# Kernel optimization log

Hardware: AMD Instinct MI355X
Metric: run time of the kernel (lower is better)

## Reference

```python
import jax, jax.numpy as jnp
import numpy as np

EMB_BOUND = 0.000316
T, E, D = 16, 100000, 128
B = 4096
L = 20  # fixed bag length used to build offsets (TBE supports ragged; math identical)


def setup_inputs() -> dict:
    key = jax.random.key(0)
    kw, ki = jax.random.split(key)
    weights = jax.random.uniform(kw, (T, E, D), dtype=jnp.float32,
                                 minval=-EMB_BOUND, maxval=EMB_BOUND)
    indices = jax.random.randint(ki, (T * B * L,), 0, E, dtype=jnp.int64)
    offsets = (jnp.arange(T * B + 1, dtype=jnp.int64) * L)
    return {"weights": weights, "indices": indices, "offsets": offsets}


def reference(weights, indices, offsets):
    # weights: [T, E, D]; indices: [N] flat; offsets: [T*B+1], table-major bags.
    n = indices.shape[0]
    num_bags = offsets.shape[0] - 1  # T*B
    b = num_bags // T
    # bag (segment) id for each lookup index
    seg = jnp.searchsorted(offsets, jnp.arange(n, dtype=offsets.dtype), side='right') - 1
    table = seg // b  # which table each lookup belongs to
    flat_w = weights.reshape(T * E, D)
    rows = flat_w[table * E + indices]  # [N, D] irregular gather
    pooled = jax.ops.segment_sum(rows, seg, num_segments=num_bags)  # [T*B, D]
    # table-major -> [B, T*D]
    return pooled.reshape(T, b, D).transpose(1, 0, 2).reshape(b, T * D)
```

## Files before the change

### kernel.cpp

```cpp
#include <hip/hip_runtime.h>


constexpr int T = 16;
constexpr int E = 100000;
constexpr int D = 128;
constexpr int BAGS_PER_TABLE = 4096;
constexpr int NUM_BAGS = T * BAGS_PER_TABLE;
constexpr int WAVES_PER_BLOCK = 4;

__global__ __launch_bounds__(256) void tbe_pool_kernel(
    const float* __restrict__ weights,
    const int* __restrict__ indices,
    const int* __restrict__ offsets,
    float* __restrict__ out)
{
    const int wave = threadIdx.x >> 6;
    const int lane = threadIdx.x & 63;
    const int bag  = blockIdx.x * WAVES_PER_BLOCK + wave;
    if (bag >= NUM_BAGS) return;

    const int t = bag / BAGS_PER_TABLE;
    const int b = bag - t * BAGS_PER_TABLE;

    const int start = offsets[bag];
    const int end   = offsets[bag + 1];

    const float2* __restrict__ tbl =
        reinterpret_cast<const float2*>(weights + (long long)t * E * D);

    float2 a0 = {0.f, 0.f}, a1 = {0.f, 0.f}, a2 = {0.f, 0.f}, a3 = {0.f, 0.f};

    int i = start;
    for (; i + 4 <= end; i += 4) {
        const int i0 = indices[i];
        const int i1 = indices[i + 1];
        const int i2 = indices[i + 2];
        const int i3 = indices[i + 3];
        const float2 v0 = tbl[(long long)i0 * (D / 2) + lane];
        const float2 v1 = tbl[(long long)i1 * (D / 2) + lane];
        const float2 v2 = tbl[(long long)i2 * (D / 2) + lane];
        const float2 v3 = tbl[(long long)i3 * (D / 2) + lane];
        a0.x += v0.x; a0.y += v0.y;
        a1.x += v1.x; a1.y += v1.y;
        a2.x += v2.x; a2.y += v2.y;
        a3.x += v3.x; a3.y += v3.y;
    }
    for (; i < end; ++i) {
        const int i0 = indices[i];
        const float2 v0 = tbl[(long long)i0 * (D / 2) + lane];
        a0.x += v0.x; a0.y += v0.y;
    }

    float2 acc;
    acc.x = (a0.x + a1.x) + (a2.x + a3.x);
    acc.y = (a0.y + a1.y) + (a2.y + a3.y);

    float2* __restrict__ o =
        reinterpret_cast<float2*>(out + (long long)b * (T * D) + t * D);
    o[lane] = acc;
}

extern "C" void kernel_launch(void* const* d_in, const int* in_sizes, int n_in,
                              void* d_out, int out_size, void* d_ws, size_t ws_size,
                              hipStream_t stream) {
    const float* weights = (const float*)d_in[0];
    const int*   indices = (const int*)d_in[1];
    const int*   offsets = (const int*)d_in[2];
    float*       out     = (float*)d_out;

    const int grid = NUM_BAGS / WAVES_PER_BLOCK;
    tbe_pool_kernel<<<grid, 256, 0, stream>>>(weights, indices, offsets, out);
}
```

Baseline: 969.8 us.

## Gather two rows per wave with 16-byte loads and shuffle-broadcast indices

Each wave now splits into two 32-lane halves, and each half gathers a different embedding row with 16-byte vector loads, so one wave instruction fetches two rows. Bag indices are read cooperatively once per 64 and broadcast with shuffles instead of per-lane scalar loads. The halves are combined with a cross-half shuffle reduction, and output is written with nontemporal stores. Row offsets use 32-bit unsigned byte arithmetic, which fits within one table, in exchange for the extra shuffle work and reduction.

```diff
diff --git a/kernel.cpp b/kernel.cpp
--- a/kernel.cpp
+++ b/kernel.cpp
@@ -7,6 +7,10 @@
 constexpr int BAGS_PER_TABLE = 4096;
 constexpr int NUM_BAGS = T * BAGS_PER_TABLE;
 constexpr int WAVES_PER_BLOCK = 4;
+constexpr int BLOCKS_PER_TABLE = BAGS_PER_TABLE / WAVES_PER_BLOCK;
+static_assert(BAGS_PER_TABLE % WAVES_PER_BLOCK == 0, "table must be block-aligned");
+
+typedef float f4 __attribute__((ext_vector_type(4)));
 
 __global__ __launch_bounds__(256) void tbe_pool_kernel(
     const float* __restrict__ weights,
@@ -16,48 +20,69 @@
 {
     const int wave = threadIdx.x >> 6;
     const int lane = threadIdx.x & 63;
-    const int bag  = blockIdx.x * WAVES_PER_BLOCK + wave;
-    if (bag >= NUM_BAGS) return;
+    const int half = lane >> 5;
+    const int l32  = lane & 31;
 
-    const int t = bag / BAGS_PER_TABLE;
-    const int b = bag - t * BAGS_PER_TABLE;
+    const int t            = blockIdx.x / BLOCKS_PER_TABLE;
+    const int bag_in_table = (blockIdx.x % BLOCKS_PER_TABLE) * WAVES_PER_BLOCK + wave;
+    const int bag          = t * BAGS_PER_TABLE + bag_in_table;
 
     const int start = offsets[bag];
     const int end   = offsets[bag + 1];
 
-    const float2* __restrict__ tbl =
-        reinterpret_cast<const float2*>(weights + (long long)t * E * D);
+    const char* __restrict__ tbl =
+        reinterpret_cast<const char*>(weights) + (size_t)t * E * D * sizeof(float);
+    const unsigned laneByte = (unsigned)(l32 * 16);
 
-    float2 a0 = {0.f, 0.f}, a1 = {0.f, 0.f}, a2 = {0.f, 0.f}, a3 = {0.f, 0.f};
+    f4 a0 = {0.f, 0.f, 0.f, 0.f};
+    f4 a1 = {0.f, 0.f, 0.f, 0.f};
+    f4 a2 = {0.f, 0.f, 0.f, 0.f};
+    f4 a3 = {0.f, 0.f, 0.f, 0.f};
 
-    int i = start;
-    for (; i + 4 <= end; i += 4) {
-        const int i0 = indices[i];
-        const int i1 = indices[i + 1];
-        const int i2 = indices[i + 2];
-        const int i3 = indices[i + 3];
-        const float2 v0 = tbl[(long long)i0 * (D / 2) + lane];
-        const float2 v1 = tbl[(long long)i1 * (D / 2) + lane];
-        const float2 v2 = tbl[(long long)i2 * (D / 2) + lane];
-        const float2 v3 = tbl[(long long)i3 * (D / 2) + lane];
-        a0.x += v0.x; a0.y += v0.y;
-        a1.x += v1.x; a1.y += v1.y;
-        a2.x += v2.x; a2.y += v2.y;
-        a3.x += v3.x; a3.y += v3.y;
-    }
-    for (; i < end; ++i) {
-        const int i0 = indices[i];
-        const float2 v0 = tbl[(long long)i0 * (D / 2) + lane];
-        a0.x += v0.x; a0.y += v0.y;
+    for (int base = start; base < end; base += 64) {
+        const int navail = min(64, end - base);
+
+        int myidx = 0;
+        if (lane < navail) myidx = indices[base + lane];
+
+        const int npairs = navail >> 1;
+        int p = 0;
+        for (; p + 4 <= npairs; p += 4) {
+            const int r0 = __shfl(myidx, 2 * (p + 0) + half);
+            const int r1 = __shfl(myidx, 2 * (p + 1) + half);
+            const int r2 = __shfl(myidx, 2 * (p + 2) + half);
+            const int r3 = __shfl(myidx, 2 * (p + 3) + half);
+            const f4 v0 = *reinterpret_cast<const f4*>(tbl + ((unsigned)r0 * 512u + laneByte));
+            const f4 v1 = *reinterpret_cast<const f4*>(tbl + ((unsigned)r1 * 512u + laneByte));
+            const f4 v2 = *reinterpret_cast<const f4*>(tbl + ((unsigned)r2 * 512u + laneByte));
+            const f4 v3 = *reinterpret_cast<const f4*>(tbl + ((unsigned)r3 * 512u + laneByte));
+            a0 += v0; a1 += v1; a2 += v2; a3 += v3;
+        }
+        for (; p < npairs; ++p) {
+            const int r0 = __shfl(myidx, 2 * p + half);
+            const f4 v0 = *reinterpret_cast<const f4*>(tbl + ((unsigned)r0 * 512u + laneByte));
+            a0 += v0;
+        }
+        if (navail & 1) {
+            const int r0 = __shfl(myidx, navail - 1);
+            if (half == 0) {
+                const f4 v0 = *reinterpret_cast<const f4*>(tbl + ((unsigned)r0 * 512u + laneByte));
+                a0 += v0;
+            }
+        }
     }
 
-    float2 acc;
-    acc.x = (a0.x + a1.x) + (a2.x + a3.x);
-    acc.y = (a0.y + a1.y) + (a2.y + a3.y);
+    f4 acc = (a0 + a1) + (a2 + a3);
+    acc.x += __shfl_xor(acc.x, 32);
+    acc.y += __shfl_xor(acc.y, 32);
+    acc.z += __shfl_xor(acc.z, 32);
+    acc.w += __shfl_xor(acc.w, 32);
 
-    float2* __restrict__ o =
-        reinterpret_cast<float2*>(out + (long long)b * (T * D) + t * D);
-    o[lane] = acc;
+    if (half == 0) {
+        f4* __restrict__ o = reinterpret_cast<f4*>(
+            out + (size_t)bag_in_table * (T * D) + (size_t)t * D);
+        __builtin_nontemporal_store(acc, o + l32);
+    }
 }
 
 extern "C" void kernel_launch(void* const* d_in, const int* in_sizes, int n_in,
```

After: 972.3 us. About the same (+0.3%).
